# Kernel optimization log

Hardware: AMD Instinct MI355X
Metric: run time of the kernel (lower is better)

The kernel has to match this reference:

```python
import jax, jax.numpy as jnp
import numpy as np

DIM = 512
RANK = 64


def setup_inputs() -> dict:
    key = jax.random.key(0)
    ks = jax.random.split(key, 8)
    B, T, S = 2, 1024, 1024
    target_val = jax.random.normal(ks[0], (B, T, DIM), dtype=jnp.float32)
    source_val = jax.random.normal(ks[1], (B, S, DIM), dtype=jnp.float32)
    # Linear weights stored torch-style [out, in]
    Wt = jax.random.normal(ks[2], (RANK, DIM), dtype=jnp.float32) / np.sqrt(DIM)
    Ws = jax.random.normal(ks[3], (RANK, DIM), dtype=jnp.float32) / np.sqrt(DIM)
    wt_out = jax.random.normal(ks[4], (RANK,), dtype=jnp.float32) / np.sqrt(RANK)
    ws_out = jax.random.normal(ks[5], (RANK,), dtype=jnp.float32) / np.sqrt(RANK)
    interaction_weight = 0.02 * jax.random.normal(ks[6], (RANK,), dtype=jnp.float32)
    bias = jnp.zeros((), dtype=jnp.float32)
    return {
        'target_val': target_val,
        'source_val': source_val,
        'Wt': Wt,
        'Ws': Ws,
        'wt_out': wt_out,
        'ws_out': ws_out,
        'interaction_weight': interaction_weight,
        'bias': bias,
    }


def reference(target_val, source_val, Wt, Ws, wt_out, ws_out, interaction_weight, bias):
    # Project to low-rank width r
    pt = jnp.einsum('btd,rd->btr', target_val, Wt)   # [B,T,R]
    ps = jnp.einsum('bsd,rd->bsr', source_val, Ws)   # [B,S,R]
    target_linear = jnp.einsum('btr,r->bt', pt, wt_out)  # [B,T]
    source_linear = jnp.einsum('bsr,r->bs', ps, ws_out)  # [B,S]
    # Pairwise multiplicative interaction -> SiLU -> rank reduction
    interaction = jax.nn.silu(pt[:, :, None, :] * ps[:, None, :, :])  # [B,T,S,R]
    scores = jnp.einsum('btsr,r->bts', interaction, interaction_weight)
    scores = scores + target_linear[:, :, None] + source_linear[:, None, :] + bias
    return scores
```

## Files before the change

kernel.cpp:

```cpp
#include <hip/hip_runtime.h>

#define DIM   512
#define RANK  64
#define TDIM  1024
#define BB    2
#define NROWS (BB * TDIM)

typedef float v4f __attribute__((ext_vector_type(4)));

__device__ __forceinline__ float fast_exp2(float x) { return __builtin_amdgcn_exp2f(x); }
__device__ __forceinline__ float fast_rcp(float x)  { return __builtin_amdgcn_rcpf(x); }

__global__ __launch_bounds__(256)
void proj_kernel(const float* __restrict__ tv, const float* __restrict__ sv,
                 const float* __restrict__ Wt, const float* __restrict__ Ws,
                 float* __restrict__ pt, float* __restrict__ ps)
{
    const int which = blockIdx.z;
    const float* X = which ? sv : tv;
    const float* W = which ? Ws : Wt;
    float* P       = which ? ps : pt;

    const int row0 = blockIdx.x * 64;
    const int kc   = blockIdx.y * 64;
    const int tid  = threadIdx.x;
    const int tx   = tid & 15;
    const int ty   = tid >> 4;

    __shared__ float xs[64][68];
    __shared__ float wsm[64][68];

#pragma unroll
    for (int p = 0; p < 4; p++) {
        const int r = (tid >> 4) + p * 16;
        const int c = (tid & 15) * 4;
        *(v4f*)&xs[r][c]  = *(const v4f*)&X[(size_t)(row0 + r) * DIM + kc + c];
        *(v4f*)&wsm[r][c] = *(const v4f*)&W[(size_t)r * DIM + kc + c];
    }
    __syncthreads();

    float acc[4][4];
#pragma unroll
    for (int i = 0; i < 4; i++)
#pragma unroll
        for (int j = 0; j < 4; j++) acc[i][j] = 0.f;

#pragma unroll 2
    for (int k4 = 0; k4 < 64; k4 += 4) {
        v4f a[4], b[4];
#pragma unroll
        for (int i = 0; i < 4; i++) a[i] = *(const v4f*)&xs[ty + 16 * i][k4];
#pragma unroll
        for (int j = 0; j < 4; j++) b[j] = *(const v4f*)&wsm[tx + 16 * j][k4];
#pragma unroll
        for (int i = 0; i < 4; i++)
#pragma unroll
            for (int j = 0; j < 4; j++) {
                acc[i][j] = fmaf(a[i].x, b[j].x, acc[i][j]);
                acc[i][j] = fmaf(a[i].y, b[j].y, acc[i][j]);
                acc[i][j] = fmaf(a[i].z, b[j].z, acc[i][j]);
                acc[i][j] = fmaf(a[i].w, b[j].w, acc[i][j]);
            }
    }

#pragma unroll
    for (int i = 0; i < 4; i++)
#pragma unroll
        for (int j = 0; j < 4; j++)
            atomicAdd(&P[(size_t)(row0 + ty + 16 * i) * RANK + tx + 16 * j], acc[i][j]);
}

__global__ __launch_bounds__(256)
void pair_kernel(const float* __restrict__ pt, const float* __restrict__ ps,
                 const float* __restrict__ wt_out, const float* __restrict__ ws_out,
                 const float* __restrict__ iw, const float* __restrict__ bias_p,
                 float* __restrict__ out)
{
    const int b  = blockIdx.z;
    const int t0 = blockIdx.y * 32;
    const int s0 = blockIdx.x * 64;
    const int tid = threadIdx.x;
    const int tx  = tid & 15;
    const int ty  = tid >> 4;

    __shared__ float pts[32][68];
    __shared__ float sts[64][68];
    __shared__ __align__(16) float wsh[64];
    __shared__ float tlsh[32];
    __shared__ float slsh[64];

    const float* ptb = pt + ((size_t)b * TDIM + t0) * RANK;
    const float* psb = ps + ((size_t)b * TDIM + s0) * RANK;

#pragma unroll
    for (int p = 0; p < 2; p++) {
        const int r = (tid >> 4) + p * 16;
        const int c = (tid & 15) * 4;
        *(v4f*)&pts[r][c] = *(const v4f*)&ptb[(size_t)r * RANK + c];
    }
#pragma unroll
    for (int p = 0; p < 4; p++) {
        const int r = (tid >> 4) + p * 16;
        const int c = (tid & 15) * 4;
        *(v4f*)&sts[r][c] = *(const v4f*)&psb[(size_t)r * RANK + c];
    }
    if (tid < 64) wsh[tid] = iw[tid];
    __syncthreads();

    if (tid < 32) {
        float v = 0.f;
#pragma unroll 8
        for (int r = 0; r < RANK; r++) v = fmaf(pts[tid][r], wt_out[r], v);
        tlsh[tid] = v;
    } else if (tid >= 64 && tid < 128) {
        const int s = tid - 64;
        float v = 0.f;
#pragma unroll 8
        for (int r = 0; r < RANK; r++) v = fmaf(sts[s][r], ws_out[r], v);
        slsh[s] = v;
    }
    __syncthreads();

    const float bias = bias_p[0];
    const float NL2E = -1.44269504088896340736f;

    float acc[2][4];
#pragma unroll
    for (int i = 0; i < 2; i++)
#pragma unroll
        for (int j = 0; j < 4; j++) acc[i][j] = 0.f;

    for (int r4 = 0; r4 < RANK; r4 += 4) {
        const v4f wv4 = *(const v4f*)&wsh[r4];
        const float wv[4] = {wv4.x, wv4.y, wv4.z, wv4.w};

        float a2[2][4], wa[2][4], bv[4][4];
#pragma unroll
        for (int i = 0; i < 2; i++) {
            const v4f av = *(const v4f*)&pts[ty + 16 * i][r4];
            const float avv[4] = {av.x, av.y, av.z, av.w};
#pragma unroll
            for (int k = 0; k < 4; k++) {
                a2[i][k] = avv[k] * NL2E;
                wa[i][k] = avv[k] * wv[k];
            }
        }
#pragma unroll
        for (int j = 0; j < 4; j++) {
            const v4f bb = *(const v4f*)&sts[tx + 16 * j][r4];
            bv[j][0] = bb.x; bv[j][1] = bb.y; bv[j][2] = bb.z; bv[j][3] = bb.w;
        }

#pragma unroll
        for (int i = 0; i < 2; i++)
#pragma unroll
            for (int j = 0; j < 4; j++)
#pragma unroll
                for (int k2 = 0; k2 < 4; k2 += 2) {
                    const float t0v = a2[i][k2]     * bv[j][k2];
                    const float t1v = a2[i][k2 + 1] * bv[j][k2 + 1];
                    const float e0  = fast_exp2(t0v);
                    const float e1  = fast_exp2(t1v);
                    const float d0  = e0 + 1.0f;
                    const float d1  = e1 + 1.0f;
                    const float r   = fast_rcp(d0 * d1);
                    const float s0  = r * d1;
                    const float s1  = r * d0;
                    const float wz0 = wa[i][k2]     * bv[j][k2];
                    const float wz1 = wa[i][k2 + 1] * bv[j][k2 + 1];
                    acc[i][j] = fmaf(wz0, s0, acc[i][j]);
                    acc[i][j] = fmaf(wz1, s1, acc[i][j]);
                }
    }

#pragma unroll
    for (int i = 0; i < 2; i++) {
        const int t = t0 + ty + 16 * i;
        const float tl = tlsh[ty + 16 * i];
        float* orow = out + ((size_t)b * TDIM + t) * TDIM + s0;
#pragma unroll
        for (int j = 0; j < 4; j++) {
            orow[tx + 16 * j] = acc[i][j] + tl + slsh[tx + 16 * j] + bias;
        }
    }
}

extern "C" void kernel_launch(void* const* d_in, const int* in_sizes, int n_in,
                              void* d_out, int out_size, void* d_ws, size_t ws_size,
                              hipStream_t stream)
{
    const float* tv     = (const float*)d_in[0];
    const float* sv     = (const float*)d_in[1];
    const float* Wt     = (const float*)d_in[2];
    const float* Ws     = (const float*)d_in[3];
    const float* wt_out = (const float*)d_in[4];
    const float* ws_out = (const float*)d_in[5];
    const float* iw     = (const float*)d_in[6];
    const float* bias   = (const float*)d_in[7];
    float* out = (float*)d_out;

    float* pt = (float*)d_ws;
    float* ps = pt + (size_t)NROWS * RANK;

    hipMemsetAsync(d_ws, 0, 2 * (size_t)NROWS * RANK * sizeof(float), stream);

    dim3 pgrid(NROWS / 64, DIM / 64, 2);
    proj_kernel<<<pgrid, 256, 0, stream>>>(tv, sv, Wt, Ws, pt, ps);

    dim3 ggrid(TDIM / 64, TDIM / 32, BB);
    pair_kernel<<<ggrid, 256, 0, stream>>>(pt, ps, wt_out, ws_out, iw, bias, out);
}
```

Measured before the change: 115.7 us.

## Replace split-K atomic projection with full-K double-buffered tiles and drop memset

The projection kernel now walks the full 512-wide reduction inside each block, using double-buffered shared-memory tiles and register prefetch. Results are written directly instead of accumulated with atomics. This removes the workspace memset launch and the atomic traffic. In exchange there are fewer blocks (128 instead of 512) with a longer serial loop, which may reduce parallelism.

Result: slower. 118.5 us (+2.4%).

```diff
diff --git a/kernel.cpp b/kernel.cpp
--- a/kernel.cpp
+++ b/kernel.cpp
@@ -21,53 +21,83 @@
     const float* W = which ? Ws : Wt;
     float* P       = which ? ps : pt;
 
-    const int row0 = blockIdx.x * 64;
-    const int kc   = blockIdx.y * 64;
+    const int row0 = blockIdx.x * 32;
     const int tid  = threadIdx.x;
     const int tx   = tid & 15;
     const int ty   = tid >> 4;
 
-    __shared__ float xs[64][68];
-    __shared__ float wsm[64][68];
-
-#pragma unroll
-    for (int p = 0; p < 4; p++) {
-        const int r = (tid >> 4) + p * 16;
-        const int c = (tid & 15) * 4;
-        *(v4f*)&xs[r][c]  = *(const v4f*)&X[(size_t)(row0 + r) * DIM + kc + c];
-        *(v4f*)&wsm[r][c] = *(const v4f*)&W[(size_t)r * DIM + kc + c];
-    }
+    __shared__ float xs[2][32][68];
+    __shared__ float wsm[2][64][68];
+
+    const int lr = tid >> 4;
+    const int lc = (tid & 15) * 4;
+
+#pragma unroll
+    for (int p = 0; p < 2; p++)
+        *(v4f*)&xs[0][lr + 16 * p][lc] =
+            *(const v4f*)&X[(size_t)(row0 + lr + 16 * p) * DIM + lc];
+#pragma unroll
+    for (int p = 0; p < 4; p++)
+        *(v4f*)&wsm[0][lr + 16 * p][lc] =
+            *(const v4f*)&W[(size_t)(lr + 16 * p) * DIM + lc];
     __syncthreads();
 
-    float acc[4][4];
-#pragma unroll
-    for (int i = 0; i < 4; i++)
+    float acc[2][4];
+#pragma unroll
+    for (int i = 0; i < 2; i++)
 #pragma unroll
         for (int j = 0; j < 4; j++) acc[i][j] = 0.f;
 
+    int buf = 0;
+    for (int kc = 0; kc < DIM; kc += 64) {
+        v4f xpre[2], wpre[4];
+        const bool more = (kc + 64) < DIM;
+        if (more) {
+            const int koff = kc + 64 + lc;
+#pragma unroll
+            for (int p = 0; p < 2; p++)
+                xpre[p] = *(const v4f*)&X[(size_t)(row0 + lr + 16 * p) * DIM + koff];
+#pragma unroll
+            for (int p = 0; p < 4; p++)
+                wpre[p] = *(const v4f*)&W[(size_t)(lr + 16 * p) * DIM + koff];
+        }
+
 #pragma unroll 2
-    for (int k4 = 0; k4 < 64; k4 += 4) {
-        v4f a[4], b[4];
-#pragma unroll
-        for (int i = 0; i < 4; i++) a[i] = *(const v4f*)&xs[ty + 16 * i][k4];
-#pragma unroll
-        for (int j = 0; j < 4; j++) b[j] = *(const v4f*)&wsm[tx + 16 * j][k4];
-#pragma unroll
-        for (int i = 0; i < 4; i++)
-#pragma unroll
-            for (int j = 0; j < 4; j++) {
-                acc[i][j] = fmaf(a[i].x, b[j].x, acc[i][j]);
-                acc[i][j] = fmaf(a[i].y, b[j].y, acc[i][j]);
-                acc[i][j] = fmaf(a[i].z, b[j].z, acc[i][j]);
-                acc[i][j] = fmaf(a[i].w, b[j].w, acc[i][j]);
-            }
-    }
-
-#pragma unroll
-    for (int i = 0; i < 4; i++)
+        for (int k4 = 0; k4 < 64; k4 += 4) {
+            v4f a[2], b[4];
+#pragma unroll
+            for (int i = 0; i < 2; i++)
+                a[i] = *(const v4f*)&xs[buf][ty + 16 * i][k4];
+#pragma unroll
+            for (int j = 0; j < 4; j++)
+                b[j] = *(const v4f*)&wsm[buf][tx + 16 * j][k4];
+#pragma unroll
+            for (int i = 0; i < 2; i++)
+#pragma unroll
+                for (int j = 0; j < 4; j++) {
+                    acc[i][j] = fmaf(a[i].x, b[j].x, acc[i][j]);
+                    acc[i][j] = fmaf(a[i].y, b[j].y, acc[i][j]);
+                    acc[i][j] = fmaf(a[i].z, b[j].z, acc[i][j]);
+                    acc[i][j] = fmaf(a[i].w, b[j].w, acc[i][j]);
+                }
+        }
+
+        if (more) {
+            const int nxt = buf ^ 1;
+#pragma unroll
+            for (int p = 0; p < 2; p++) *(v4f*)&xs[nxt][lr + 16 * p][lc] = xpre[p];
+#pragma unroll
+            for (int p = 0; p < 4; p++) *(v4f*)&wsm[nxt][lr + 16 * p][lc] = wpre[p];
+        }
+        __syncthreads();
+        buf ^= 1;
+    }
+
+#pragma unroll
+    for (int i = 0; i < 2; i++)
 #pragma unroll
         for (int j = 0; j < 4; j++)
-            atomicAdd(&P[(size_t)(row0 + ty + 16 * i) * RANK + tx + 16 * j], acc[i][j]);
+            P[(size_t)(row0 + ty + 16 * i) * RANK + tx + 16 * j] = acc[i][j];
 }
 
 __global__ __launch_bounds__(256)
@@ -202,9 +232,7 @@
     float* pt = (float*)d_ws;
     float* ps = pt + (size_t)NROWS * RANK;
 
-    hipMemsetAsync(d_ws, 0, 2 * (size_t)NROWS * RANK * sizeof(float), stream);
-
-    dim3 pgrid(NROWS / 64, DIM / 64, 2);
+    dim3 pgrid(NROWS / 32, 1, 2);
     proj_kernel<<<pgrid, 256, 0, stream>>>(tv, sv, Wt, Ws, pt, ps);
 
     dim3 ggrid(TDIM / 64, TDIM / 32, BB);
```

## Replace atomic split-K projection with partial buffers and pack pair-kernel math

Applied to the files above, without the earlier changes.

The projection kernel now splits K into four chunks that write plain vectorized partial results to separate workspace slices, which removes the memset and the atomics. The pair kernel sums the four partials when it loads its tiles. The rank dimension is permuted so each thread's stored columns line up, and the projection weights are kept in shared memory. The sigmoid pair math is reworked to use one reciprocal per four terms and packed 2-wide float ops, at the cost of extra partial-sum reads and a product of four denominators that could overflow when exponents are large.

Result: faster. 112.3 us, median of 2 (-2.9%).

```diff
diff --git a/kernel.cpp b/kernel.cpp
--- a/kernel.cpp
+++ b/kernel.cpp
@@ -1,12 +1,15 @@
 #include <hip/hip_runtime.h>
 
-#define DIM   512
-#define RANK  64
-#define TDIM  1024
-#define BB    2
-#define NROWS (BB * TDIM)
+#define DIM    512
+#define RANK   64
+#define TDIM   1024
+#define BB     2
+#define NROWS  (BB * TDIM)
+#define KSPLIT 4
+#define KCH    (DIM / KSPLIT)
 
 typedef float v4f __attribute__((ext_vector_type(4)));
+typedef float v2f __attribute__((ext_vector_type(2)));
 
 __device__ __forceinline__ float fast_exp2(float x) { return __builtin_amdgcn_exp2f(x); }
 __device__ __forceinline__ float fast_rcp(float x)  { return __builtin_amdgcn_rcpf(x); }
@@ -19,41 +22,50 @@
     const int which = blockIdx.z;
     const float* X = which ? sv : tv;
     const float* W = which ? Ws : Wt;
-    float* P       = which ? ps : pt;
-
-    const int row0 = blockIdx.x * 64;
-    const int kc   = blockIdx.y * 64;
+    float* P = (which ? ps : pt) + (size_t)blockIdx.y * NROWS * RANK;
+
+    const int row0 = blockIdx.x * 32;
+    const int kc   = blockIdx.y * KCH;
     const int tid  = threadIdx.x;
     const int tx   = tid & 15;
     const int ty   = tid >> 4;
 
-    __shared__ float xs[64][68];
-    __shared__ float wsm[64][68];
+    __shared__ float xs[32][132];
+    __shared__ float wsm[64][132];
 
 #pragma unroll
     for (int p = 0; p < 4; p++) {
-        const int r = (tid >> 4) + p * 16;
-        const int c = (tid & 15) * 4;
-        *(v4f*)&xs[r][c]  = *(const v4f*)&X[(size_t)(row0 + r) * DIM + kc + c];
+        const int li = p * 256 + tid;
+        const int r  = li >> 5;
+        const int c  = (li & 31) << 2;
+        *(v4f*)&xs[r][c] = *(const v4f*)&X[(size_t)(row0 + r) * DIM + kc + c];
+    }
+#pragma unroll
+    for (int p = 0; p < 8; p++) {
+        const int li = p * 256 + tid;
+        const int r  = li >> 5;
+        const int c  = (li & 31) << 2;
         *(v4f*)&wsm[r][c] = *(const v4f*)&W[(size_t)r * DIM + kc + c];
     }
     __syncthreads();
 
-    float acc[4][4];
-#pragma unroll
-    for (int i = 0; i < 4; i++)
+    float acc[2][4];
+#pragma unroll
+    for (int i = 0; i < 2; i++)
 #pragma unroll
         for (int j = 0; j < 4; j++) acc[i][j] = 0.f;
 
-#pragma unroll 2
-    for (int k4 = 0; k4 < 64; k4 += 4) {
-        v4f a[4], b[4];
-#pragma unroll
-        for (int i = 0; i < 4; i++) a[i] = *(const v4f*)&xs[ty + 16 * i][k4];
-#pragma unroll
-        for (int j = 0; j < 4; j++) b[j] = *(const v4f*)&wsm[tx + 16 * j][k4];
-#pragma unroll
-        for (int i = 0; i < 4; i++)
+#pragma unroll 4
+    for (int k4 = 0; k4 < KCH; k4 += 4) {
+        v4f a[2], b[4];
+#pragma unroll
+        for (int i = 0; i < 2; i++)
+            a[i] = *(const v4f*)&xs[ty + 16 * i][k4];
+#pragma unroll
+        for (int j = 0; j < 4; j++)
+            b[j] = *(const v4f*)&wsm[tx + 16 * j][k4];
+#pragma unroll
+        for (int i = 0; i < 2; i++)
 #pragma unroll
             for (int j = 0; j < 4; j++) {
                 acc[i][j] = fmaf(a[i].x, b[j].x, acc[i][j]);
@@ -64,10 +76,10 @@
     }
 
 #pragma unroll
-    for (int i = 0; i < 4; i++)
-#pragma unroll
-        for (int j = 0; j < 4; j++)
-            atomicAdd(&P[(size_t)(row0 + ty + 16 * i) * RANK + tx + 16 * j], acc[i][j]);
+    for (int i = 0; i < 2; i++) {
+        v4f o = {acc[i][0], acc[i][1], acc[i][2], acc[i][3]};
+        *(v4f*)&P[(size_t)(row0 + ty + 16 * i) * RANK + tx * 4] = o;
+    }
 }
 
 __global__ __launch_bounds__(256)
@@ -86,37 +98,57 @@
     __shared__ float pts[32][68];
     __shared__ float sts[64][68];
     __shared__ __align__(16) float wsh[64];
+    __shared__ float wtsh[64];
+    __shared__ float wssh[64];
     __shared__ float tlsh[32];
     __shared__ float slsh[64];
 
+    const size_t SPL = (size_t)NROWS * RANK;
     const float* ptb = pt + ((size_t)b * TDIM + t0) * RANK;
     const float* psb = ps + ((size_t)b * TDIM + s0) * RANK;
 
 #pragma unroll
     for (int p = 0; p < 2; p++) {
-        const int r = (tid >> 4) + p * 16;
-        const int c = (tid & 15) * 4;
-        *(v4f*)&pts[r][c] = *(const v4f*)&ptb[(size_t)r * RANK + c];
+        const int li = p * 256 + tid;
+        const int r  = li >> 4;
+        const int c  = (li & 15) << 2;
+        const float* src = ptb + (size_t)r * RANK + c;
+        v4f v = *(const v4f*)src;
+        v += *(const v4f*)(src + SPL);
+        v += *(const v4f*)(src + 2 * SPL);
+        v += *(const v4f*)(src + 3 * SPL);
+        *(v4f*)&pts[r][c] = v;
     }
 #pragma unroll
     for (int p = 0; p < 4; p++) {
-        const int r = (tid >> 4) + p * 16;
-        const int c = (tid & 15) * 4;
-        *(v4f*)&sts[r][c] = *(const v4f*)&psb[(size_t)r * RANK + c];
-    }
-    if (tid < 64) wsh[tid] = iw[tid];
+        const int li = p * 256 + tid;
+        const int r  = li >> 4;
+        const int c  = (li & 15) << 2;
+        const float* src = psb + (size_t)r * RANK + c;
+        v4f v = *(const v4f*)src;
+        v += *(const v4f*)(src + SPL);
+        v += *(const v4f*)(src + 2 * SPL);
+        v += *(const v4f*)(src + 3 * SPL);
+        *(v4f*)&sts[r][c] = v;
+    }
+    if (tid < 64) {
+        const int lg = (tid >> 2) + 16 * (tid & 3);
+        wsh[tid]  = iw[lg];
+        wtsh[tid] = wt_out[lg];
+        wssh[tid] = ws_out[lg];
+    }
     __syncthreads();
 
     if (tid < 32) {
         float v = 0.f;
 #pragma unroll 8
-        for (int r = 0; r < RANK; r++) v = fmaf(pts[tid][r], wt_out[r], v);
+        for (int r = 0; r < RANK; r++) v = fmaf(pts[tid][r], wtsh[r], v);
         tlsh[tid] = v;
     } else if (tid >= 64 && tid < 128) {
         const int s = tid - 64;
         float v = 0.f;
 #pragma unroll 8
-        for (int r = 0; r < RANK; r++) v = fmaf(sts[s][r], ws_out[r], v);
+        for (int r = 0; r < RANK; r++) v = fmaf(sts[s][r], wssh[r], v);
         slsh[s] = v;
     }
     __syncthreads();
@@ -132,45 +164,52 @@
 
     for (int r4 = 0; r4 < RANK; r4 += 4) {
         const v4f wv4 = *(const v4f*)&wsh[r4];
-        const float wv[4] = {wv4.x, wv4.y, wv4.z, wv4.w};
-
-        float a2[2][4], wa[2][4], bv[4][4];
+        const v2f wvA = {wv4.x, wv4.y};
+        const v2f wvB = {wv4.z, wv4.w};
+
+        v2f a2[2][2], wa[2][2];
 #pragma unroll
         for (int i = 0; i < 2; i++) {
             const v4f av = *(const v4f*)&pts[ty + 16 * i][r4];
-            const float avv[4] = {av.x, av.y, av.z, av.w};
-#pragma unroll
-            for (int k = 0; k < 4; k++) {
-                a2[i][k] = avv[k] * NL2E;
-                wa[i][k] = avv[k] * wv[k];
-            }
+            const v2f aA = {av.x, av.y};
+            const v2f aB = {av.z, av.w};
+            a2[i][0] = aA * NL2E;
+            a2[i][1] = aB * NL2E;
+            wa[i][0] = aA * wvA;
+            wa[i][1] = aB * wvB;
         }
+        v2f bv[4][2];
 #pragma unroll
         for (int j = 0; j < 4; j++) {
             const v4f bb = *(const v4f*)&sts[tx + 16 * j][r4];
-            bv[j][0] = bb.x; bv[j][1] = bb.y; bv[j][2] = bb.z; bv[j][3] = bb.w;
+            bv[j][0] = (v2f){bb.x, bb.y};
+            bv[j][1] = (v2f){bb.z, bb.w};
         }
 
 #pragma unroll
         for (int i = 0; i < 2; i++)
 #pragma unroll
-            for (int j = 0; j < 4; j++)
-#pragma unroll
-                for (int k2 = 0; k2 < 4; k2 += 2) {
-                    const float t0v = a2[i][k2]     * bv[j][k2];
-                    const float t1v = a2[i][k2 + 1] * bv[j][k2 + 1];
-                    const float e0  = fast_exp2(t0v);
-                    const float e1  = fast_exp2(t1v);
-                    const float d0  = e0 + 1.0f;
-                    const float d1  = e1 + 1.0f;
-                    const float r   = fast_rcp(d0 * d1);
-                    const float s0  = r * d1;
-                    const float s1  = r * d0;
-                    const float wz0 = wa[i][k2]     * bv[j][k2];
-                    const float wz1 = wa[i][k2 + 1] * bv[j][k2 + 1];
-                    acc[i][j] = fmaf(wz0, s0, acc[i][j]);
-                    acc[i][j] = fmaf(wz1, s1, acc[i][j]);
-                }
+            for (int j = 0; j < 4; j++) {
+                const v2f tA = a2[i][0] * bv[j][0];
+                const v2f tB = a2[i][1] * bv[j][1];
+                const float e0 = fast_exp2(tA.x);
+                const float e1 = fast_exp2(tA.y);
+                const float e2 = fast_exp2(tB.x);
+                const float e3 = fast_exp2(tB.y);
+                v2f dA = {e0, e1};  dA += 1.0f;
+                v2f dB = {e2, e3};  dB += 1.0f;
+                const float pA = dA.x * dA.y;
+                const float pB = dB.x * dB.y;
+                const float r  = fast_rcp(pA * pB);
+                const v2f nA = wa[i][0] * bv[j][0];
+                const v2f nB = wa[i][1] * bv[j][1];
+                const float uA = fmaf(nA.y, dA.x, nA.x * dA.y);
+                const float uB = fmaf(nB.y, dB.x, nB.x * dB.y);
+                const float rA = r * pB;
+                const float rB = r * pA;
+                acc[i][j] = fmaf(rA, uA, acc[i][j]);
+                acc[i][j] = fmaf(rB, uB, acc[i][j]);
+            }
     }
 
 #pragma unroll
@@ -199,12 +238,11 @@
     const float* bias   = (const float*)d_in[7];
     float* out = (float*)d_out;
 
+    const size_t SPL = (size_t)NROWS * RANK;
     float* pt = (float*)d_ws;
-    float* ps = pt + (size_t)NROWS * RANK;
-
-    hipMemsetAsync(d_ws, 0, 2 * (size_t)NROWS * RANK * sizeof(float), stream);
-
-    dim3 pgrid(NROWS / 64, DIM / 64, 2);
+    float* ps = pt + (size_t)KSPLIT * SPL;
+
+    dim3 pgrid(NROWS / 32, KSPLIT, 2);
     proj_kernel<<<pgrid, 256, 0, stream>>>(tv, sv, Wt, Ws, pt, ps);
 
     dim3 ggrid(TDIM / 64, TDIM / 32, BB);
```
